# Kernel tuning notes

Hardware: AMD Instinct MI355X
Metric: run time of the kernel (lower is better)

The kernel has to match this reference:

```python
import jax, jax.numpy as jnp
import numpy as np

B, N, M, C = 8, 2048, 2048, 512


def setup_inputs() -> dict:
    key = jax.random.key(0)
    ks = jax.random.split(key, 10)
    s = 1.0 / np.sqrt(C)
    dec_embed = jax.random.normal(ks[0], (B, N, C), dtype=jnp.float32)
    enc_embed = jax.random.normal(ks[1], (B, M, C), dtype=jnp.float32)
    trans_mat = (jax.random.uniform(ks[2], (B, N, M)) < 0.5).astype(jnp.float32)
    Wv = jax.random.uniform(ks[3], (C, C), minval=-s, maxval=s, dtype=jnp.float32)
    bv = jax.random.uniform(ks[4], (C,), minval=-s, maxval=s, dtype=jnp.float32)
    W1 = jax.random.uniform(ks[5], (C, C), minval=-s, maxval=s, dtype=jnp.float32)
    b1 = jax.random.uniform(ks[6], (C,), minval=-s, maxval=s, dtype=jnp.float32)
    W2 = jax.random.uniform(ks[7], (C, C), minval=-s, maxval=s, dtype=jnp.float32)
    b2 = jax.random.uniform(ks[8], (C,), minval=-s, maxval=s, dtype=jnp.float32)
    return {"dec_embed": dec_embed, "enc_embed": enc_embed, "trans_mat": trans_mat,
            "Wv": Wv, "bv": bv, "W1": W1, "b1": b1, "W2": W2, "b2": b2}


def reference(dec_embed, enc_embed, trans_mat, Wv, bv, W1, b1, W2, b2):
    # scores [B,N,M], elementwise-masked by trans_mat
    attn = jnp.einsum('bnc,bmc->bnm', dec_embed, enc_embed) * trans_mat
    # NONSTANDARD masked softmax: zeros participate in softmax (exp(0)=1 in denom),
    # then positions where attn==0 are re-zeroed.
    sm = jax.nn.softmax(attn, axis=-1)
    attn = jnp.where(attn != 0, sm, jnp.zeros((), attn.dtype))
    v = enc_embed @ Wv + bv                      # [B,M,C]
    v = jnp.tanh(jnp.einsum('bnm,bmc->bnc', attn, v))  # [B,N,C]
    g = dec_embed * v + dec_embed                # tanh-gate + residual
    h = jax.nn.relu(g @ W1 + b1)                 # Mlp fc1 + ReLU (drop=0)
    return h @ W2 + b2                           # Mlp fc2
```

## Files before the change

kernel.cpp:

```cpp
#include <hip/hip_runtime.h>
#include <math.h>

#define Bb 8
#define Nn 2048
#define Mm 2048
#define Cc 512

typedef __attribute__((ext_vector_type(8))) _Float16 hfrag;
typedef __attribute__((ext_vector_type(4))) float f4;
typedef __attribute__((ext_vector_type(4))) _Float16 h4;

__device__ __forceinline__ void gld16(const void* g, void* l) {
    __builtin_amdgcn_global_load_lds(
        (const __attribute__((address_space(1))) void*)g,
        (__attribute__((address_space(3))) void*)l, 16, 0, 0);
}

template<int EPI, int BN, int SWZ>
__global__ __launch_bounds__(256) void gemm_mfma(
    const _Float16* __restrict__ Ah, long sA, int lda,
    const _Float16* __restrict__ Bh, long sB, int ldb,
    const float* __restrict__ aux, long sAux, int ldaux,
    const _Float16* __restrict__ aux2,
    float* __restrict__ mlal,
    void* __restrict__ Cout, long sC, int ldc, int K, int GX)
{
    constexpr int NI = (BN == 128) ? 4 : 2;
    constexpr int NQ = (1024 + BN * 8) / 256;

    __shared__ _Float16 As[2 * 128 * 32];
    __shared__ _Float16 Bs[2 * BN * 32];

    int bx, by, bz;
    if (SWZ == 1) {
        const int id = blockIdx.x;
        bz = id & 7; bx = (id >> 3) % GX; by = (id >> 3) / GX;
    } else if (SWZ == 2) {
        const int id = blockIdx.x;
        bz = 0; bx = (id >> 3) % GX; by = (id & 7) + 8 * ((id >> 3) / GX);
    } else {
        bx = blockIdx.x; by = blockIdx.y; bz = 0;
    }

    const _Float16* A0 = Ah + (size_t)bz * sA;
    const _Float16* B0 = Bh + (size_t)bz * sB;

    const int tid  = threadIdx.x;
    const int wv   = tid >> 6;
    const int ln   = tid & 63;
    const int wx   = (BN == 128) ? (wv & 1) : 0;
    const int wy   = (BN == 128) ? (wv >> 1) : wv;
    const int lcol = ln & 15, quad = ln >> 4;
    const int row0w = wy * (NI * 16);
    const int col0w = wx * 64;

    const int rowBase = by * 128;
    const int colBase = bx * BN;

    f4 acc[NI][4];
    const f4 z4 = {0.f, 0.f, 0.f, 0.f};
    #pragma unroll
    for (int i = 0; i < NI; ++i)
        #pragma unroll
        for (int j = 0; j < 4; ++j) acc[i][j] = z4;

    const float* alb = (EPI == 2) ? (mlal + (size_t)bz * (2048 * 32)) : nullptr;
    _Float16 als[4] = {(_Float16)0.f, (_Float16)0.f, (_Float16)0.f, (_Float16)0.f};

    for (int k0 = 0; k0 < K; k0 += 64) {
        __syncthreads();
        #pragma unroll
        for (int q = 0; q < NQ; ++q) {
            const int c0 = q * 256 + wv * 64;
            const int c  = c0 + ln;
            if (c0 < 1024) {
                const int hh = c >> 9;
                const int r  = (c >> 2) & 127;
                const int ko = hh * 32 + (c & 3) * 8;
                gld16(A0 + (size_t)(rowBase + r) * lda + k0 + ko, &As[c0 * 8]);
            } else {
                const int cb = c - 1024;
                const int hh = cb / (BN * 4);
                const int r  = (cb >> 2) & (BN - 1);
                const int ko = hh * 32 + (cb & 3) * 8;
                gld16(B0 + (size_t)(colBase + r) * ldb + k0 + ko, &Bs[(c0 - 1024) * 8]);
            }
        }
        __syncthreads();

        if (EPI == 2) {
            const int t = k0 >> 6;
            #pragma unroll
            for (int j = 0; j < 4; ++j) {
                const int n = colBase + col0w + j * 16 + lcol;
                als[j] = (_Float16)alb[(size_t)n * 32 + t];
            }
        }

        #pragma unroll
        for (int hh = 0; hh < 2; ++hh) {
            hfrag af[NI], bf_[4];
            const int aoff = quad * 8;
            #pragma unroll
            for (int i = 0; i < NI; ++i)
                af[i]  = *(const hfrag*)&As[hh * 4096 + (row0w + i * 16 + lcol) * 32 + aoff];
            #pragma unroll
            for (int j = 0; j < 4; ++j)
                bf_[j] = *(const hfrag*)&Bs[hh * (BN * 32) + (col0w + j * 16 + lcol) * 32 + aoff];

            if (EPI == 2) {
                #pragma unroll
                for (int j = 0; j < 4; ++j) bf_[j] = bf_[j] * als[j];
            }

            #pragma unroll
            for (int i = 0; i < NI; ++i)
                #pragma unroll
                for (int j = 0; j < 4; ++j)
                    acc[i][j] = __builtin_amdgcn_mfma_f32_16x16x32_f16(af[i], bf_[j], acc[i][j], 0, 0, 0);
        }
    }

    const int crow0 = rowBase + row0w + quad * 4;
    const int ccol0 = colBase + col0w + lcol;

    if (EPI == 0) {
        _Float16* E = (_Float16*)Cout + (size_t)bz * sC;
        const float* Mk = aux + (size_t)bz * sAux;
        const int t = (rowBase + row0w) >> 6;

        f4 mk[NI];
        #pragma unroll
        for (int i = 0; i < NI; ++i)
            mk[i] = *(const f4*)(Mk + (size_t)ccol0 * ldaux + crow0 + i * 16);

        #pragma unroll
        for (int j = 0; j < 4; ++j) {
            const int n = ccol0 + j * 16;
            f4 mkn[NI];
            if (j < 3) {
                #pragma unroll
                for (int i = 0; i < NI; ++i)
                    mkn[i] = *(const f4*)(Mk + (size_t)(n + 16) * ldaux + crow0 + i * 16);
            }
            #pragma unroll
            for (int i = 0; i < NI; ++i)
                #pragma unroll
                for (int r = 0; r < 4; ++r) acc[i][j][r] *= mk[i][r];

            float mx = acc[0][j][0];
            #pragma unroll
            for (int i = 0; i < NI; ++i)
                #pragma unroll
                for (int r = 0; r < 4; ++r) mx = fmaxf(mx, acc[i][j][r]);
            mx = fmaxf(mx, __shfl_xor(mx, 16, 64));
            mx = fmaxf(mx, __shfl_xor(mx, 32, 64));
            float l0 = 0.f;
            #pragma unroll
            for (int i = 0; i < NI; ++i) {
                h4 ev;
                #pragma unroll
                for (int r = 0; r < 4; ++r) {
                    const float s = acc[i][j][r];
                    const float e = __expf(s - mx);
                    l0 += e;
                    ev[r] = (s == 0.f) ? (_Float16)0.f : (_Float16)e;
                }
                *(h4*)(E + (size_t)n * ldc + crow0 + i * 16) = ev;
            }
            l0 += __shfl_xor(l0, 16, 64);
            l0 += __shfl_xor(l0, 32, 64);
            if (quad == 0) {
                float2 p; p.x = mx; p.y = l0;
                ((float2*)mlal)[((size_t)bz * 2048 + n) * 32 + t] = p;
            }
            if (j < 3) {
                #pragma unroll
                for (int i = 0; i < NI; ++i) mk[i] = mkn[i];
            }
        }
    } else if (EPI == 1) {
        _Float16* C = (_Float16*)Cout;
        #pragma unroll
        for (int j = 0; j < 4; ++j) {
            const int col = ccol0 + j * 16;
            const float bi = aux[col];
            #pragma unroll
            for (int i = 0; i < NI; ++i) {
                const int rowb = crow0 + i * 16;
                const int bb = rowb >> 11, ml = rowb & 2047;
                h4 st;
                #pragma unroll
                for (int r = 0; r < 4; ++r) st[r] = (_Float16)(acc[i][j][r] + bi);
                *(h4*)(C + (size_t)bb * ((size_t)Cc * Mm) + (size_t)col * Mm + ml) = st;
            }
        }
    } else if (EPI == 2) {
        _Float16* C = (_Float16*)Cout + (size_t)bz * sC;
        const _Float16* Dg = aux2 + (size_t)bz * sC;
        #pragma unroll
        for (int i = 0; i < NI; ++i) {
            const int c0 = crow0 + i * 16;
            #pragma unroll
            for (int j = 0; j < 4; ++j) {
                const int n = ccol0 + j * 16;
                const h4 dv = *(const h4*)(Dg + (size_t)n * ldc + c0);
                h4 gv;
                #pragma unroll
                for (int r = 0; r < 4; ++r) {
                    const float a = acc[i][j][r];
                    const float th = 1.f - 2.f / (__expf(2.f * a) + 1.f);
                    gv[r] = (_Float16)((float)dv[r] * (1.f + th));
                }
                *(h4*)(C + (size_t)n * ldc + c0) = gv;
            }
        }
    } else if (EPI == 3) {
        _Float16* C = (_Float16*)Cout;
        #pragma unroll
        for (int i = 0; i < NI; ++i) {
            const int c0 = crow0 + i * 16;
            const f4 bi = *(const f4*)(aux + c0);
            #pragma unroll
            for (int j = 0; j < 4; ++j) {
                const int n = ccol0 + j * 16;
                h4 hv;
                #pragma unroll
                for (int r = 0; r < 4; ++r)
                    hv[r] = (_Float16)fmaxf(acc[i][j][r] + bi[r], 0.f);
                *(h4*)(C + (size_t)n * ldc + c0) = hv;
            }
        }
    } else {
        float* C = (float*)Cout;
        #pragma unroll
        for (int i = 0; i < NI; ++i) {
            const int c0 = crow0 + i * 16;
            const f4 bi = *(const f4*)(aux + c0);
            #pragma unroll
            for (int j = 0; j < 4; ++j) {
                const int n = ccol0 + j * 16;
                f4 ov;
                #pragma unroll
                for (int r = 0; r < 4; ++r) ov[r] = acc[i][j][r] + bi[r];
                *(f4*)(C + (size_t)n * ldc + c0) = ov;
            }
        }
    }
}

__global__ __launch_bounds__(64) void combine_kernel(
    const float* __restrict__ mlq, float* __restrict__ alpha)
{
    const int row = blockIdx.x * 64 + threadIdx.x;
    const float2* ml = (const float2*)mlq + (size_t)row * 32;
    float mt[32], lt[32];
    float m = -1e30f;
    #pragma unroll
    for (int t = 0; t < 32; ++t) {
        float2 p = ml[t];
        mt[t] = p.x; lt[t] = p.y;
        m = fmaxf(m, p.x);
    }
    float et[32], l = 0.f;
    #pragma unroll
    for (int t = 0; t < 32; ++t) {
        et[t] = __expf(mt[t] - m);
        l += lt[t] * et[t];
    }
    const float inv = 1.f / l;
    float* ap = alpha + (size_t)row * 32;
    #pragma unroll
    for (int t = 0; t < 32; ++t) ap[t] = et[t] * inv;
}

__global__ __launch_bounds__(256) void sconv(const float* __restrict__ x,
                                             _Float16* __restrict__ o)
{
    const size_t i = (size_t)blockIdx.x * 256 + threadIdx.x;
    f4 v = ((const f4*)x)[i];
    h4 hh;
    #pragma unroll
    for (int k = 0; k < 4; ++k) hh[k] = (_Float16)v[k];
    ((h4*)o)[i] = hh;
}

__global__ __launch_bounds__(256) void wconv(const float* s0, const float* s1, const float* s2,
                                             _Float16* d0, _Float16* d1, _Float16* d2)
{
    const float* Sm = blockIdx.z == 0 ? s0 : blockIdx.z == 1 ? s1 : s2;
    _Float16* D = blockIdx.z == 0 ? d0 : blockIdx.z == 1 ? d1 : d2;
    __shared__ float t[32][33];
    const int x = threadIdx.x & 31, y = threadIdx.x >> 5;
    const int gx = blockIdx.x * 32, gy = blockIdx.y * 32;
    #pragma unroll
    for (int yy = y; yy < 32; yy += 8)
        t[yy][x] = Sm[(size_t)(gy + yy) * 512 + gx + x];
    __syncthreads();
    #pragma unroll
    for (int yy = y; yy < 32; yy += 8)
        D[(size_t)(gx + yy) * 512 + gy + x] = (_Float16)t[x][yy];
}

extern "C" void kernel_launch(void* const* d_in, const int* in_sizes, int n_in,
                              void* d_out, int out_size, void* d_ws, size_t ws_size,
                              hipStream_t stream)
{
    const float* dec   = (const float*)d_in[0];
    const float* enc   = (const float*)d_in[1];
    const float* trans = (const float*)d_in[2];
    const float* Wv = (const float*)d_in[3];
    const float* bv = (const float*)d_in[4];
    const float* W1 = (const float*)d_in[5];
    const float* b1 = (const float*)d_in[6];
    const float* W2 = (const float*)d_in[7];
    const float* b2 = (const float*)d_in[8];

    char* ws = (char*)d_ws;
    _Float16* e     = (_Float16*)ws;
    float*    mlq   = (float*)(ws + 0x4000000);
    float*    alpha = (float*)(ws + 0x4400000);
    _Float16* dec_h = (_Float16*)(ws + 0x4600000);
    _Float16* Wvt   = (_Float16*)(ws + 0x5600000);
    _Float16* W1t   = Wvt + 262144;
    _Float16* W2t   = Wvt + 524288;
    _Float16* vT    = (_Float16*)(ws + 0x5800000);
    _Float16* g     = (_Float16*)(ws + 0x6800000);
    _Float16* h     = (_Float16*)(ws + 0x7800000);
    _Float16* enc_h = (_Float16*)d_out;

    sconv<<<dim3(8192), 256, 0, stream>>>(dec, dec_h);
    sconv<<<dim3(8192), 256, 0, stream>>>(enc, enc_h);
    wconv<<<dim3(16, 16, 3), 256, 0, stream>>>(Wv, W1, W2, Wvt, W1t, W2t);

    gemm_mfma<0, 128, 1><<<dim3(2048), 256, 0, stream>>>(
        enc_h, (long)Mm * Cc, 512,
        dec_h, (long)Nn * Cc, 512,
        trans, (long)Nn * Mm, 2048, nullptr, mlq,
        e, (long)Nn * Mm, 2048, 512, 16);

    combine_kernel<<<dim3(256), 64, 0, stream>>>(mlq, alpha);

    gemm_mfma<1, 64, 2><<<dim3(1024), 256, 0, stream>>>(
        enc_h, 0, 512, Wvt, 0, 512, bv, 0, 0, nullptr, nullptr,
        vT, 0, 0, 512, 8);

    gemm_mfma<2, 128, 1><<<dim3(512), 256, 0, stream>>>(
        vT, (long)Cc * Mm, 2048,
        e, (long)Nn * Mm, 2048,
        nullptr, 0, 512, dec_h, alpha,
        g, (long)Nn * Cc, 512, 2048, 16);

    gemm_mfma<3, 64, 0><<<dim3(256, 4), 256, 0, stream>>>(
        W1t, 0, 512, g, 0, 512, b1, 0, 0, nullptr, nullptr,
        h, 0, 512, 512, 0);

    gemm_mfma<4, 64, 0><<<dim3(256, 4), 256, 0, stream>>>(
        W2t, 0, 512, h, 0, 512, b2, 0, 0, nullptr, nullptr,
        d_out, 0, 512, 512, 0);
}
```

Measured before the change: 436.4 us.

## Double-buffer GEMM LDS tiles with XOR swizzle and per-32 K stages

Restructures the MFMA GEMM main loop so each iteration issues async global-to-LDS loads for the next 32-wide K slice into the other buffer while computing on the current one. This overlaps memory latency with MFMA work. It also applies an XOR swizzle to the LDS layout to reduce bank conflicts on fragment reads. The trade-offs are a smaller K step per barrier and the risk of a race, since the async global_load_lds may not be complete at the single barrier without an explicit vmcnt wait.

```diff
diff --git a/kernel.cpp b/kernel.cpp
--- a/kernel.cpp
+++ b/kernel.cpp
@@ -25,11 +25,13 @@
     float* __restrict__ mlal,
     void* __restrict__ Cout, long sC, int ldc, int K, int GX)
 {
-    constexpr int NI = (BN == 128) ? 4 : 2;
-    constexpr int NQ = (1024 + BN * 8) / 256;
-
-    __shared__ _Float16 As[2 * 128 * 32];
-    __shared__ _Float16 Bs[2 * BN * 32];
+    constexpr int NI  = (BN == 128) ? 4 : 2;
+    constexpr int ASL = 512;
+    constexpr int BSL = BN * 4;
+    constexpr int NQ  = (ASL + BSL) / 256;
+
+    __shared__ _Float16 As[2][128 * 32];
+    __shared__ _Float16 Bs[2][BN * 32];
 
     int bx, by, bz;
     if (SWZ == 1) {
@@ -57,6 +59,8 @@
     const int rowBase = by * 128;
     const int colBase = bx * BN;
 
+    const int soff = (quad ^ ((lcol >> 1) & 3)) * 8;
+
     f4 acc[NI][4];
     const f4 z4 = {0.f, 0.f, 0.f, 0.f};
     #pragma unroll
@@ -67,58 +71,60 @@
     const float* alb = (EPI == 2) ? (mlal + (size_t)bz * (2048 * 32)) : nullptr;
     _Float16 als[4] = {(_Float16)0.f, (_Float16)0.f, (_Float16)0.f, (_Float16)0.f};
 
-    for (int k0 = 0; k0 < K; k0 += 64) {
-        __syncthreads();
+    auto STAGE = [&](int k0, int p) {
         #pragma unroll
         for (int q = 0; q < NQ; ++q) {
-            const int c0 = q * 256 + wv * 64;
-            const int c  = c0 + ln;
-            if (c0 < 1024) {
-                const int hh = c >> 9;
-                const int r  = (c >> 2) & 127;
-                const int ko = hh * 32 + (c & 3) * 8;
-                gld16(A0 + (size_t)(rowBase + r) * lda + k0 + ko, &As[c0 * 8]);
+            const int c = q * 256 + wv * 64 + ln;
+            if (c < ASL) {
+                const int r = c >> 2;
+                const int g = (c & 3) ^ ((c >> 3) & 3);
+                gld16(A0 + (size_t)(rowBase + r) * lda + k0 + g * 8, &As[p][c * 8]);
             } else {
-                const int cb = c - 1024;
-                const int hh = cb / (BN * 4);
-                const int r  = (cb >> 2) & (BN - 1);
-                const int ko = hh * 32 + (cb & 3) * 8;
-                gld16(B0 + (size_t)(colBase + r) * ldb + k0 + ko, &Bs[(c0 - 1024) * 8]);
-            }
-        }
-        __syncthreads();
-
-        if (EPI == 2) {
-            const int t = k0 >> 6;
+                const int cb = c - ASL;
+                const int r  = cb >> 2;
+                const int g  = (cb & 3) ^ ((cb >> 3) & 3);
+                gld16(B0 + (size_t)(colBase + r) * ldb + k0 + g * 8, &Bs[p][cb * 8]);
+            }
+        }
+    };
+
+    const int NT = K >> 5;
+    STAGE(0, 0);
+    __syncthreads();
+
+    for (int t = 0; t < NT; ++t) {
+        const int p = t & 1;
+        if (t + 1 < NT) STAGE((t + 1) * 32, p ^ 1);
+
+        if (EPI == 2 && (t & 1) == 0) {
+            const int tt = t >> 1;
             #pragma unroll
             for (int j = 0; j < 4; ++j) {
                 const int n = colBase + col0w + j * 16 + lcol;
-                als[j] = (_Float16)alb[(size_t)n * 32 + t];
-            }
-        }
-
-        #pragma unroll
-        for (int hh = 0; hh < 2; ++hh) {
-            hfrag af[NI], bf_[4];
-            const int aoff = quad * 8;
-            #pragma unroll
-            for (int i = 0; i < NI; ++i)
-                af[i]  = *(const hfrag*)&As[hh * 4096 + (row0w + i * 16 + lcol) * 32 + aoff];
+                als[j] = (_Float16)alb[(size_t)n * 32 + tt];
+            }
+        }
+
+        hfrag af[NI], bf_[4];
+        #pragma unroll
+        for (int i = 0; i < NI; ++i)
+            af[i]  = *(const hfrag*)&As[p][(row0w + i * 16 + lcol) * 32 + soff];
+        #pragma unroll
+        for (int j = 0; j < 4; ++j)
+            bf_[j] = *(const hfrag*)&Bs[p][(col0w + j * 16 + lcol) * 32 + soff];
+
+        if (EPI == 2) {
+            #pragma unroll
+            for (int j = 0; j < 4; ++j) bf_[j] = bf_[j] * als[j];
+        }
+
+        #pragma unroll
+        for (int i = 0; i < NI; ++i)
             #pragma unroll
             for (int j = 0; j < 4; ++j)
-                bf_[j] = *(const hfrag*)&Bs[hh * (BN * 32) + (col0w + j * 16 + lcol) * 32 + aoff];
-
-            if (EPI == 2) {
-                #pragma unroll
-                for (int j = 0; j < 4; ++j) bf_[j] = bf_[j] * als[j];
-            }
-
-            #pragma unroll
-            for (int i = 0; i < NI; ++i)
-                #pragma unroll
-                for (int j = 0; j < 4; ++j)
-                    acc[i][j] = __builtin_amdgcn_mfma_f32_16x16x32_f16(af[i], bf_[j], acc[i][j], 0, 0, 0);
-        }
+                acc[i][j] = __builtin_amdgcn_mfma_f32_16x16x32_f16(af[i], bf_[j], acc[i][j], 0, 0, 0);
+
+        if (t + 1 < NT) __syncthreads();
     }
 
     const int crow0 = rowBase + row0w + quad * 4;
```

Measured after the change: 451.5 us. 3.5% more time.
